# Kernel tuning notes

Hardware: AMD Instinct MI355X
Metric: run time of the kernel (lower is better)

## Reference

```python
import jax, jax.numpy as jnp
import numpy as np

B, N, DIN, DOUT, RATIO, K = 8, 4096, 128, 256, 4, 16
S = N // RATIO
BN_EPS = 1e-5


def furthest_point_sample(xyz, n_samples):
    # xyz: [B, N, 3] -> idx [B, n_samples] int32. Sequential farthest-distance reduction.
    b, n, _ = xyz.shape
    dist0 = jnp.full((b, n), 1e10, xyz.dtype)
    last0 = xyz[:, 0, :]  # first sampled point is index 0 (CUDA kernel convention)

    def step(carry, _):
        dist, last = carry
        d = jnp.sum((xyz - last[:, None, :]) ** 2, axis=-1)  # [B, N]
        dist = jnp.minimum(dist, d)
        nxt = jnp.argmax(dist, axis=1).astype(jnp.int32)      # [B]
        last = jnp.take_along_axis(xyz, nxt[:, None, None].astype(jnp.int32), axis=1)[:, 0, :]
        return (dist, last), nxt

    (_, _), idxs = jax.lax.scan(step, (dist0, last0), None, length=n_samples - 1)
    idx = jnp.concatenate([jnp.zeros((1, b), jnp.int32), idxs], axis=0).T  # [B, S]
    return idx


def knn_indices(query, points, k):
    # query [B,S,3], points [B,N,3] -> k nearest indices [B,S,k]
    q2 = jnp.sum(query ** 2, axis=-1)                           # [B,S]
    p2 = jnp.sum(points ** 2, axis=-1)                          # [B,N]
    d2 = q2[:, :, None] + p2[:, None, :] - 2.0 * jnp.einsum('bsd,bnd->bsn', query, points)
    _, idx = jax.lax.top_k(-d2, k)                              # smallest distances
    return idx


def setup_inputs() -> dict:
    key = jax.random.key(0)
    k1, k2, k3, k4 = jax.random.split(key, 4)
    input_feature = jax.random.normal(k1, (B, N, DIN), dtype=jnp.float32)
    xyz = jax.random.uniform(k2, (B, N, 3), dtype=jnp.float32)
    # linear params (torch nn.Linear: W [out,in], b [out])
    lim = 1.0 / np.sqrt(DIN)
    W = jax.random.uniform(k3, (DOUT, DIN), dtype=jnp.float32, minval=-lim, maxval=lim)
    b = jax.random.uniform(k4, (DOUT,), dtype=jnp.float32, minval=-lim, maxval=lim)
    gamma = jnp.ones((DOUT,), jnp.float32)
    beta = jnp.zeros((DOUT,), jnp.float32)
    return {"input_feature": input_feature, "xyz": xyz, "W": W, "b": b, "gamma": gamma, "beta": beta}


def reference(input_feature, xyz, W, b, gamma, beta):
    sample_idx = furthest_point_sample(xyz, S)                         # [B,S]
    sample_xyz = jnp.take_along_axis(xyz, sample_idx[:, :, None], axis=1)  # [B,S,3]
    knn_idx = knn_indices(sample_xyz, xyz, K)                          # [B,S,K]
    # gather_knn: [B,S,K,DIN]
    knn_feat = jax.vmap(lambda f, i: f[i])(input_feature, knn_idx)
    h = jnp.einsum('bskd,ed->bske', knn_feat, W) + b                   # linear [B,S,K,DOUT]
    # BatchNorm1d over channel dim, stats across (B, S*K) in training mode (biased var)
    mean = jnp.mean(h, axis=(0, 1, 2))
    var = jnp.var(h, axis=(0, 1, 2))
    h = gamma * (h - mean) * jax.lax.rsqrt(var + BN_EPS) + beta
    h = jax.nn.relu(h)
    sample_feature = jnp.max(h, axis=2)                                # [B,S,DOUT]
    return sample_feature, sample_xyz
```

## Files before the change

kernel.cpp:

```cpp
#include <hip/hip_runtime.h>
#include <hip/hip_bf16.h>

#define BB 8
#define NN 4096
#define DIN 128
#define DOUT 256
#define SS 1024
#define KK 16

__device__ float g_g[(size_t)BB * NN * DOUT];
__device__ int   g_knn[BB * SS * KK];
__device__ int   g_wcount[BB * NN];
__device__ float g_S1[DOUT];
__device__ float g_S2[DOUT];

typedef float f32x2 __attribute__((ext_vector_type(2)));

__device__ __forceinline__ unsigned long long umax64(unsigned long long a, unsigned long long b) {
    return a > b ? a : b;
}
__device__ __forceinline__ f32x2 pk_add(f32x2 a, f32x2 b) {
    f32x2 d; asm("v_pk_add_f32 %0, %1, %2" : "=v"(d) : "v"(a), "v"(b)); return d;
}
__device__ __forceinline__ f32x2 pk_mul(f32x2 a, f32x2 b) {
    f32x2 d; asm("v_pk_mul_f32 %0, %1, %2" : "=v"(d) : "v"(a), "v"(b)); return d;
}
__device__ __forceinline__ f32x2 pk_fma(f32x2 a, f32x2 b, f32x2 c) {
    f32x2 d; asm("v_pk_fma_f32 %0, %1, %2, %3" : "=v"(d) : "v"(a), "v"(b), "v"(c)); return d;
}

__global__ __launch_bounds__(512) void k_fused1(
    const float* __restrict__ feat, const float* __restrict__ xyz,
    const float* __restrict__ W, const float* __restrict__ bias,
    float* __restrict__ out)
{
    __shared__ __align__(16) float smem[16384];
    __shared__ __align__(16) unsigned long long swk64[2][8];

    if (blockIdx.x < BB) {
        #pragma clang fp contract(off)
        const int b = blockIdx.x, tid = threadIdx.x;
        const float* bx = xyz + (size_t)b * NN * 3;
        for (int i = 0; i < 8; ++i) {
            int p = tid + i * 512;
            float4 v; v.x = bx[p*3]; v.y = bx[p*3+1]; v.z = bx[p*3+2]; v.w = 0.f;
            ((float4*)smem)[p] = v;
        }
        __syncthreads();
        f32x2 px2[4], py2[4], pz2[4];
        double dist64[8];
        float thr[8];
        unsigned long long key[8];
        const int gbase = tid * 8;
        const unsigned long long D0 =
            ((unsigned long long)__double_as_longlong(1e10)) & ~0xFFFULL;
        const float THR0 = __uint_as_float(__float_as_uint(1e10f) + 16u);
        #pragma unroll
        for (int pp = 0; pp < 4; ++pp) {
            float4 v0 = ((float4*)smem)[gbase + 2*pp];
            float4 v1 = ((float4*)smem)[gbase + 2*pp + 1];
            px2[pp].x = v0.x; px2[pp].y = v1.x;
            py2[pp].x = v0.y; py2[pp].y = v1.y;
            pz2[pp].x = v0.z; pz2[pp].y = v1.z;
            dist64[2*pp]   = 1e10; dist64[2*pp+1] = 1e10;
            thr[2*pp] = THR0;      thr[2*pp+1] = THR0;
            key[2*pp]   = D0 | (unsigned long long)(4095 - (gbase + 2*pp));
            key[2*pp+1] = D0 | (unsigned long long)(4095 - (gbase + 2*pp + 1));
        }
        float4 c0v = ((float4*)smem)[0];
        float lxf = c0v.x, lyf = c0v.y, lzf = c0v.z;
        float* oxyz = out + (size_t)BB * SS * DOUT;
        if (tid == 0) {
            oxyz[(size_t)(b*SS)*3]   = lxf;
            oxyz[(size_t)(b*SS)*3+1] = lyf;
            oxyz[(size_t)(b*SS)*3+2] = lzf;
        }
        for (int s = 1; s < SS; ++s) {
            const double lxd = (double)lxf, lyd = (double)lyf, lzd = (double)lzf;
            f32x2 nlx; nlx.x = -lxf; nlx.y = -lxf;
            f32x2 nly; nly.x = -lyf; nly.y = -lyf;
            f32x2 nlz; nlz.x = -lzf; nlz.y = -lzf;
            #pragma unroll
            for (int pp = 0; pp < 4; ++pp) {
                f32x2 dx = pk_add(px2[pp], nlx);
                f32x2 dy = pk_add(py2[pp], nly);
                f32x2 dz = pk_add(pz2[pp], nlz);
                f32x2 d2 = pk_mul(dx, dx);
                d2 = pk_fma(dy, dy, d2);
                d2 = pk_fma(dz, dz, d2);
                if (d2.x < thr[2*pp]) {
                    const int r = 2*pp;
                    double ddx = (double)px2[pp].x - lxd;
                    double ddy = (double)py2[pp].x - lyd;
                    double ddz = (double)pz2[pp].x - lzd;
                    double m1 = ddx*ddx, m2 = ddy*ddy, m3 = ddz*ddz;
                    double d = (m1 + m2) + m3;
                    if (d < dist64[r]) {
                        dist64[r] = d;
                        thr[r] = __uint_as_float(__float_as_uint((float)d) + 16u);
                        key[r] = (((unsigned long long)__double_as_longlong(d)) & ~0xFFFULL)
                                 | (unsigned long long)(4095 - (gbase + r));
                    }
                }
                if (d2.y < thr[2*pp+1]) {
                    const int r = 2*pp + 1;
                    double ddx = (double)px2[pp].y - lxd;
                    double ddy = (double)py2[pp].y - lyd;
                    double ddz = (double)pz2[pp].y - lzd;
                    double m1 = ddx*ddx, m2 = ddy*ddy, m3 = ddz*ddz;
                    double d = (m1 + m2) + m3;
                    if (d < dist64[r]) {
                        dist64[r] = d;
                        thr[r] = __uint_as_float(__float_as_uint((float)d) + 16u);
                        key[r] = (((unsigned long long)__double_as_longlong(d)) & ~0xFFFULL)
                                 | (unsigned long long)(4095 - (gbase + r));
                    }
                }
            }
            unsigned long long kk;
            {
                unsigned long long a0 = umax64(key[0], key[1]);
                unsigned long long a1 = umax64(key[2], key[3]);
                unsigned long long a2 = umax64(key[4], key[5]);
                unsigned long long a3 = umax64(key[6], key[7]);
                kk = umax64(umax64(a0, a1), umax64(a2, a3));
            }
#define DPP64(CTRL) { \
    int _lo = __builtin_amdgcn_update_dpp(0, (int)(unsigned)kk, CTRL, 0xf, 0xf, true); \
    int _hi = __builtin_amdgcn_update_dpp(0, (int)(unsigned)(kk >> 32), CTRL, 0xf, 0xf, true); \
    unsigned long long _o = (((unsigned long long)(unsigned)_hi) << 32) | (unsigned)_lo; \
    if (_o > kk) kk = _o; }
            DPP64(0x111)
            DPP64(0x112)
            DPP64(0x114)
            DPP64(0x118)
            DPP64(0x142)
            DPP64(0x143)
#undef DPP64
            if ((tid & 63) == 63) swk64[s & 1][tid >> 6] = kk;
            __syncthreads();
            const unsigned long long* sw = swk64[s & 1];
            ulonglong2 s01 = ((const ulonglong2*)sw)[0];
            ulonglong2 s23 = ((const ulonglong2*)sw)[1];
            ulonglong2 s45 = ((const ulonglong2*)sw)[2];
            ulonglong2 s67 = ((const ulonglong2*)sw)[3];
            unsigned long long kmax = umax64(
                umax64(umax64(s01.x, s01.y), umax64(s23.x, s23.y)),
                umax64(umax64(s45.x, s45.y), umax64(s67.x, s67.y)));
            int widx = 4095 - (int)(kmax & 0xFFFULL);
            float4 c = ((float4*)smem)[widx];
            lxf = c.x; lyf = c.y; lzf = c.z;
            if (tid == 0) {
                oxyz[(size_t)(b*SS+s)*3]   = c.x;
                oxyz[(size_t)(b*SS+s)*3+1] = c.y;
                oxyz[(size_t)(b*SS+s)*3+2] = c.z;
            }
        }
    } else if (blockIdx.x < BB + 2048) {
        int gi = blockIdx.x - BB;
        int mt = gi & 511, nt = gi >> 9;
        int rbase = mt * 64, cbase = nt * 64;
        float* As = smem;
        float* Bs = smem + 64 * 36;
        int tid = threadIdx.x;
        int tx = tid & 15, ty = tid >> 4;
        int c0 = tx * 4, r0 = ty * 2;
        int lr = tid >> 3;
        int lk = (tid & 7) * 4;
        float acc[2][4] = {{0.f,0.f,0.f,0.f},{0.f,0.f,0.f,0.f}};
        for (int kc = 0; kc < 4; ++kc) {
            __syncthreads();
            float4 av = *(const float4*)&feat[(size_t)(rbase + lr) * DIN + kc*32 + lk];
            *(float4*)&As[lr * 36 + lk] = av;
            float4 wv = *(const float4*)&W[(size_t)(cbase + lr) * DIN + kc*32 + lk];
            Bs[(lk+0)*68 + lr] = wv.x;
            Bs[(lk+1)*68 + lr] = wv.y;
            Bs[(lk+2)*68 + lr] = wv.z;
            Bs[(lk+3)*68 + lr] = wv.w;
            __syncthreads();
            const float* Ar0 = &As[r0 * 36];
            const float* Ar1 = Ar0 + 36;
            #pragma unroll
            for (int k = 0; k < 32; ++k) {
                float a0 = Ar0[k], a1 = Ar1[k];
                float4 bv = *(float4*)&Bs[k * 68 + c0];
                acc[0][0] += a0 * bv.x; acc[0][1] += a0 * bv.y;
                acc[0][2] += a0 * bv.z; acc[0][3] += a0 * bv.w;
                acc[1][0] += a1 * bv.x; acc[1][1] += a1 * bv.y;
                acc[1][2] += a1 * bv.z; acc[1][3] += a1 * bv.w;
            }
        }
        float4 bb4 = *(const float4*)&bias[cbase + c0];
        float4 o0, o1;
        o0.x = acc[0][0] + bb4.x; o0.y = acc[0][1] + bb4.y;
        o0.z = acc[0][2] + bb4.z; o0.w = acc[0][3] + bb4.w;
        o1.x = acc[1][0] + bb4.x; o1.y = acc[1][1] + bb4.y;
        o1.z = acc[1][2] + bb4.z; o1.w = acc[1][3] + bb4.w;
        *(float4*)&g_g[(size_t)(rbase + r0)     * DOUT + cbase + c0] = o0;
        *(float4*)&g_g[(size_t)(rbase + r0 + 1) * DOUT + cbase + c0] = o1;
    } else {
        int zi = blockIdx.x - (BB + 2048);
        int t = zi * 512 + threadIdx.x;
        g_wcount[t] = 0;
        g_wcount[t + 16384] = 0;
        if (t < DOUT) { g_S1[t] = 0.f; g_S2[t] = 0.f; }
    }
}

__global__ __launch_bounds__(1024) void k_knn(
    const float* __restrict__ xyz, const float* __restrict__ out)
{
    __shared__ __align__(16) float4 pts[NN];
    __shared__ unsigned hist[16][512];
    __shared__ int cand[16][128];
    __shared__ int cnt[16];
    const int tid = threadIdx.x, lane = tid & 63, w = tid >> 6;
    const int q = blockIdx.x * 16 + w;
    const int b = blockIdx.x >> 6;
    const float* bx = xyz + (size_t)b * NN * 3;
    for (int i = 0; i < 4; ++i) {
        int p = tid + i * 1024;
        float4 v; v.x = bx[p*3]; v.y = bx[p*3+1]; v.z = bx[p*3+2]; v.w = 0.f;
        pts[p] = v;
    }
    { unsigned* h = &hist[0][0];
      #pragma unroll
      for (int i = 0; i < 8; ++i) h[tid + i * 1024] = 0u; }
    if (tid < 16) cnt[tid] = 0;
    __syncthreads();

    const float* sx = out + (size_t)BB * SS * DOUT + (size_t)q * 3;
    const float qxf = sx[0], qyf = sx[1], qzf = sx[2];
    unsigned minub = 0xFFFFFFFFu;
    for (int t = 0; t < 64; ++t) {
        int n = t * 64 + lane;
        float4 p = pts[n];
        float dx = qxf - p.x, dy = qyf - p.y, dz = qzf - p.z;
        float df = fmaf(dz, dz, fmaf(dy, dy, dx * dx));
        unsigned ub = __float_as_uint(df);
        minub = ub < minub ? ub : minub;
        unsigned bk = ub < 0x30800000u ? 0u : ((ub - 0x30800000u) >> 19);
        bk = bk > 511u ? 511u : bk;
        atomicAdd(&hist[w][bk], 1u);
    }
    #pragma unroll
    for (int m = 1; m < 64; m <<= 1) {
        unsigned o = __shfl_xor(minub, m);
        minub = o < minub ? o : minub;
    }
    unsigned mb = minub < 0x30800000u ? 0u : ((minub - 0x30800000u) >> 19);
    mb = mb > 511u ? 511u : mb;
    int Tb = 511;
    unsigned base = 0;
    for (int ch = (int)(mb >> 6); ch < 8; ++ch) {
        unsigned v = hist[w][ch * 64 + lane];
        #pragma unroll
        for (int m = 1; m < 64; m <<= 1) {
            unsigned t2 = __shfl_up(v, m);
            if (lane >= m) v += t2;
        }
        unsigned tot = __shfl(v, 63);
        unsigned long long msk = __ballot(base + v >= 16u);
        if (msk) { Tb = ch * 64 + (__ffsll(msk) - 1); break; }
        base += tot;
    }
    unsigned Tcap = (unsigned)Tb + 1u; Tcap = Tcap > 511u ? 511u : Tcap;
    for (int t = 0; t < 64; ++t) {
        int n = t * 64 + lane;
        float4 p = pts[n];
        float dx = qxf - p.x, dy = qyf - p.y, dz = qzf - p.z;
        float df = fmaf(dz, dz, fmaf(dy, dy, dx * dx));
        unsigned ub = __float_as_uint(df);
        unsigned bk = ub < 0x30800000u ? 0u : ((ub - 0x30800000u) >> 19);
        bk = bk > 511u ? 511u : bk;
        if (bk <= Tcap) {
            int slot = atomicAdd(&cnt[w], 1);
            if (slot < 128) cand[w][slot] = n;
        }
    }
    {
        #pragma clang fp contract(off)
        int count = cnt[w]; count = count > 128 ? 128 : count;
        const double qx = (double)qxf, qy = (double)qyf, qz = (double)qzf;
        int i0 = lane < count ? cand[w][lane] : -1;
        int i1 = (lane + 64) < count ? cand[w][lane + 64] : -1;
        double d0 = 1e300, d1 = 1e300;
        if (i0 >= 0) {
            float4 p = pts[i0];
            double dx = qx - (double)p.x, dy = qy - (double)p.y, dz = qz - (double)p.z;
            double m1 = dx*dx, m2 = dy*dy, m3 = dz*dz;
            d0 = (m1 + m2) + m3;
        }
        if (i1 >= 0) {
            float4 p = pts[i1];
            double dx = qx - (double)p.x, dy = qy - (double)p.y, dz = qz - (double)p.z;
            double m1 = dx*dx, m2 = dy*dy, m3 = dz*dz;
            d1 = (m1 + m2) + m3;
        }
        int r0 = 0, r1 = 0;
        for (int i = 0; i < count; ++i) {
            double od; int oi;
            if (i < 64) { od = __shfl(d0, i);      oi = __shfl(i0, i); }
            else        { od = __shfl(d1, i - 64); oi = __shfl(i1, i - 64); }
            if ((od < d0) || (od == d0 && oi < i0)) ++r0;
            if ((od < d1) || (od == d1 && oi < i1)) ++r1;
        }
        if (i0 >= 0 && r0 < KK) {
            g_knn[(size_t)q * KK + r0] = i0;
            atomicAdd(&g_wcount[b * NN + i0], 1);
        }
        if (i1 >= 0 && r1 < KK) {
            g_knn[(size_t)q * KK + r1] = i1;
            atomicAdd(&g_wcount[b * NN + i1], 1);
        }
    }
}

__global__ __launch_bounds__(256) void k_stats()
{
    int tid = threadIdx.x;
    int rbase = blockIdx.x * 128;
    float a1 = 0.f, a2 = 0.f;
    for (int i = 0; i < 128; ++i) {
        int row = rbase + i;
        int w = g_wcount[row];
        if (w) {
            float v = g_g[(size_t)row * DOUT + tid];
            float wf = (float)w;
            a1 += wf * v;
            a2 += wf * v * v;
        }
    }
    atomicAdd(&g_S1[tid], a1);
    atomicAdd(&g_S2[tid], a2);
}

__global__ __launch_bounds__(256) void k_final(
    const float* __restrict__ gamma, const float* __restrict__ beta,
    float* __restrict__ out)
{
    int w = threadIdx.x >> 6, lane = threadIdx.x & 63;
    int q = blockIdx.x * 4 + w;
    int b = q >> 10;
    int c = lane * 4;
    const int* ki = g_knn + (size_t)q * KK;
    float4 m; m.x = m.y = m.z = m.w = -1e30f;
    for (int k = 0; k < KK; ++k) {
        int idx = ki[k];
        float4 v = *(const float4*)&g_g[((size_t)(b * NN + idx)) * DOUT + c];
        m.x = fmaxf(m.x, v.x); m.y = fmaxf(m.y, v.y);
        m.z = fmaxf(m.z, v.z); m.w = fmaxf(m.w, v.w);
    }
    const float inv = 1.0f / 131072.0f;
    float4 s1 = *(const float4*)&g_S1[c];
    float4 s2 = *(const float4*)&g_S2[c];
    float4 ga = *(const float4*)&gamma[c];
    float4 be = *(const float4*)&beta[c];
    float4 o;
    {
        float mean = s1.x * inv; float var = s2.x * inv - mean * mean;
        float rs = rsqrtf(var + 1e-5f);
        float t = ga.x * (m.x - mean); t = t * rs; t += be.x; o.x = fmaxf(t, 0.f);
    }
    {
        float mean = s1.y * inv; float var = s2.y * inv - mean * mean;
        float rs = rsqrtf(var + 1e-5f);
        float t = ga.y * (m.y - mean); t = t * rs; t += be.y; o.y = fmaxf(t, 0.f);
    }
    {
        float mean = s1.z * inv; float var = s2.z * inv - mean * mean;
        float rs = rsqrtf(var + 1e-5f);
        float t = ga.z * (m.z - mean); t = t * rs; t += be.z; o.z = fmaxf(t, 0.f);
    }
    {
        float mean = s1.w * inv; float var = s2.w * inv - mean * mean;
        float rs = rsqrtf(var + 1e-5f);
        float t = ga.w * (m.w - mean); t = t * rs; t += be.w; o.w = fmaxf(t, 0.f);
    }
    *(float4*)&out[(size_t)q * DOUT + c] = o;
}

extern "C" void kernel_launch(void* const* d_in, const int* in_sizes, int n_in,
                              void* d_out, int out_size, void* d_ws, size_t ws_size,
                              hipStream_t stream) {
    (void)in_sizes; (void)n_in; (void)out_size; (void)d_ws; (void)ws_size;
    const float* feat  = (const float*)d_in[0];
    const float* xyz   = (const float*)d_in[1];
    const float* W     = (const float*)d_in[2];
    const float* bias  = (const float*)d_in[3];
    const float* gamma = (const float*)d_in[4];
    const float* beta  = (const float*)d_in[5];
    float* out = (float*)d_out;

    k_fused1<<<BB + 2048 + 32, 512, 0, stream>>>(feat, xyz, W, bias, out);
    k_knn   <<<BB * SS / 16, 1024, 0, stream>>>(xyz, out);
    k_stats <<<256, 256, 0, stream>>>();
    k_final <<<2048, 256, 0, stream>>>(gamma, beta, out);
}
```

Baseline: 1.012 ms.

## Widen FPS blocks to 1024 threads with four points per thread

```diff
diff --git a/kernel.cpp b/kernel.cpp
--- a/kernel.cpp
+++ b/kernel.cpp
@@ -28,35 +28,38 @@
 __device__ __forceinline__ f32x2 pk_fma(f32x2 a, f32x2 b, f32x2 c) {
     f32x2 d; asm("v_pk_fma_f32 %0, %1, %2, %3" : "=v"(d) : "v"(a), "v"(b), "v"(c)); return d;
 }
-
-__global__ __launch_bounds__(512) void k_fused1(
+__device__ __forceinline__ void lgkm_barrier() {
+    asm volatile("s_waitcnt lgkmcnt(0)\n\ts_barrier" ::: "memory");
+}
+
+__global__ __launch_bounds__(1024) void k_fused1(
     const float* __restrict__ feat, const float* __restrict__ xyz,
     const float* __restrict__ W, const float* __restrict__ bias,
     float* __restrict__ out)
 {
     __shared__ __align__(16) float smem[16384];
-    __shared__ __align__(16) unsigned long long swk64[2][8];
+    __shared__ __align__(16) unsigned long long swk64[2][16];
 
     if (blockIdx.x < BB) {
         #pragma clang fp contract(off)
         const int b = blockIdx.x, tid = threadIdx.x;
         const float* bx = xyz + (size_t)b * NN * 3;
-        for (int i = 0; i < 8; ++i) {
-            int p = tid + i * 512;
+        for (int i = 0; i < 4; ++i) {
+            int p = tid + i * 1024;
             float4 v; v.x = bx[p*3]; v.y = bx[p*3+1]; v.z = bx[p*3+2]; v.w = 0.f;
             ((float4*)smem)[p] = v;
         }
         __syncthreads();
-        f32x2 px2[4], py2[4], pz2[4];
-        double dist64[8];
-        float thr[8];
-        unsigned long long key[8];
-        const int gbase = tid * 8;
+        f32x2 px2[2], py2[2], pz2[2];
+        double dist64[4];
+        float thr[4];
+        unsigned long long key[4];
+        const int gbase = tid * 4;
         const unsigned long long D0 =
             ((unsigned long long)__double_as_longlong(1e10)) & ~0xFFFULL;
         const float THR0 = __uint_as_float(__float_as_uint(1e10f) + 16u);
         #pragma unroll
-        for (int pp = 0; pp < 4; ++pp) {
+        for (int pp = 0; pp < 2; ++pp) {
             float4 v0 = ((float4*)smem)[gbase + 2*pp];
             float4 v1 = ((float4*)smem)[gbase + 2*pp + 1];
             px2[pp].x = v0.x; px2[pp].y = v1.x;
@@ -76,12 +79,13 @@
             oxyz[(size_t)(b*SS)*3+2] = lzf;
         }
         for (int s = 1; s < SS; ++s) {
+            const int sl = s & 1;
             const double lxd = (double)lxf, lyd = (double)lyf, lzd = (double)lzf;
             f32x2 nlx; nlx.x = -lxf; nlx.y = -lxf;
             f32x2 nly; nly.x = -lyf; nly.y = -lyf;
             f32x2 nlz; nlz.x = -lzf; nlz.y = -lzf;
             #pragma unroll
-            for (int pp = 0; pp < 4; ++pp) {
+            for (int pp = 0; pp < 2; ++pp) {
                 f32x2 dx = pk_add(px2[pp], nlx);
                 f32x2 dy = pk_add(py2[pp], nly);
                 f32x2 dz = pk_add(pz2[pp], nlz);
@@ -117,14 +121,8 @@
                     }
                 }
             }
-            unsigned long long kk;
-            {
-                unsigned long long a0 = umax64(key[0], key[1]);
-                unsigned long long a1 = umax64(key[2], key[3]);
-                unsigned long long a2 = umax64(key[4], key[5]);
-                unsigned long long a3 = umax64(key[6], key[7]);
-                kk = umax64(umax64(a0, a1), umax64(a2, a3));
-            }
+            unsigned long long kk = umax64(umax64(key[0], key[1]),
+                                           umax64(key[2], key[3]));
 #define DPP64(CTRL) { \
     int _lo = __builtin_amdgcn_update_dpp(0, (int)(unsigned)kk, CTRL, 0xf, 0xf, true); \
     int _hi = __builtin_amdgcn_update_dpp(0, (int)(unsigned)(kk >> 32), CTRL, 0xf, 0xf, true); \
@@ -137,16 +135,22 @@
             DPP64(0x142)
             DPP64(0x143)
 #undef DPP64
-            if ((tid & 63) == 63) swk64[s & 1][tid >> 6] = kk;
-            __syncthreads();
-            const unsigned long long* sw = swk64[s & 1];
-            ulonglong2 s01 = ((const ulonglong2*)sw)[0];
-            ulonglong2 s23 = ((const ulonglong2*)sw)[1];
-            ulonglong2 s45 = ((const ulonglong2*)sw)[2];
-            ulonglong2 s67 = ((const ulonglong2*)sw)[3];
-            unsigned long long kmax = umax64(
-                umax64(umax64(s01.x, s01.y), umax64(s23.x, s23.y)),
-                umax64(umax64(s45.x, s45.y), umax64(s67.x, s67.y)));
+            if ((tid & 63) == 63) swk64[sl][tid >> 6] = kk;
+            lgkm_barrier();
+            const unsigned long long* sw = swk64[sl];
+            ulonglong2 q0 = ((const ulonglong2*)sw)[0];
+            ulonglong2 q1 = ((const ulonglong2*)sw)[1];
+            ulonglong2 q2 = ((const ulonglong2*)sw)[2];
+            ulonglong2 q3 = ((const ulonglong2*)sw)[3];
+            ulonglong2 q4 = ((const ulonglong2*)sw)[4];
+            ulonglong2 q5 = ((const ulonglong2*)sw)[5];
+            ulonglong2 q6 = ((const ulonglong2*)sw)[6];
+            ulonglong2 q7 = ((const ulonglong2*)sw)[7];
+            unsigned long long m0 = umax64(umax64(q0.x, q0.y), umax64(q1.x, q1.y));
+            unsigned long long m1 = umax64(umax64(q2.x, q2.y), umax64(q3.x, q3.y));
+            unsigned long long m2 = umax64(umax64(q4.x, q4.y), umax64(q5.x, q5.y));
+            unsigned long long m3 = umax64(umax64(q6.x, q6.y), umax64(q7.x, q7.y));
+            unsigned long long kmax = umax64(umax64(m0, m1), umax64(m2, m3));
             int widx = 4095 - (int)(kmax & 0xFFFULL);
             float4 c = ((float4*)smem)[widx];
             lxf = c.x; lyf = c.y; lzf = c.z;
@@ -163,46 +167,52 @@
         float* As = smem;
         float* Bs = smem + 64 * 36;
         int tid = threadIdx.x;
-        int tx = tid & 15, ty = tid >> 4;
+        bool active = tid < 512;
+        int tx = tid & 15, ty = (tid & 511) >> 4;
         int c0 = tx * 4, r0 = ty * 2;
-        int lr = tid >> 3;
+        int lr = (tid & 511) >> 3;
         int lk = (tid & 7) * 4;
         float acc[2][4] = {{0.f,0.f,0.f,0.f},{0.f,0.f,0.f,0.f}};
         for (int kc = 0; kc < 4; ++kc) {
             __syncthreads();
-            float4 av = *(const float4*)&feat[(size_t)(rbase + lr) * DIN + kc*32 + lk];
-            *(float4*)&As[lr * 36 + lk] = av;
-            float4 wv = *(const float4*)&W[(size_t)(cbase + lr) * DIN + kc*32 + lk];
-            Bs[(lk+0)*68 + lr] = wv.x;
-            Bs[(lk+1)*68 + lr] = wv.y;
-            Bs[(lk+2)*68 + lr] = wv.z;
-            Bs[(lk+3)*68 + lr] = wv.w;
+            if (active) {
+                float4 av = *(const float4*)&feat[(size_t)(rbase + lr) * DIN + kc*32 + lk];
+                *(float4*)&As[lr * 36 + lk] = av;
+                float4 wv = *(const float4*)&W[(size_t)(cbase + lr) * DIN + kc*32 + lk];
+                Bs[(lk+0)*68 + lr] = wv.x;
+                Bs[(lk+1)*68 + lr] = wv.y;
+                Bs[(lk+2)*68 + lr] = wv.z;
+                Bs[(lk+3)*68 + lr] = wv.w;
+            }
             __syncthreads();
-            const float* Ar0 = &As[r0 * 36];
-            const float* Ar1 = Ar0 + 36;
-            #pragma unroll
-            for (int k = 0; k < 32; ++k) {
-                float a0 = Ar0[k], a1 = Ar1[k];
-                float4 bv = *(float4*)&Bs[k * 68 + c0];
-                acc[0][0] += a0 * bv.x; acc[0][1] += a0 * bv.y;
-                acc[0][2] += a0 * bv.z; acc[0][3] += a0 * bv.w;
-                acc[1][0] += a1 * bv.x; acc[1][1] += a1 * bv.y;
-                acc[1][2] += a1 * bv.z; acc[1][3] += a1 * bv.w;
+            if (active) {
+                const float* Ar0 = &As[r0 * 36];
+                const float* Ar1 = Ar0 + 36;
+                #pragma unroll
+                for (int k = 0; k < 32; ++k) {
+                    float a0 = Ar0[k], a1 = Ar1[k];
+                    float4 bv = *(float4*)&Bs[k * 68 + c0];
+                    acc[0][0] += a0 * bv.x; acc[0][1] += a0 * bv.y;
+                    acc[0][2] += a0 * bv.z; acc[0][3] += a0 * bv.w;
+                    acc[1][0] += a1 * bv.x; acc[1][1] += a1 * bv.y;
+                    acc[1][2] += a1 * bv.z; acc[1][3] += a1 * bv.w;
+                }
             }
         }
-        float4 bb4 = *(const float4*)&bias[cbase + c0];
-        float4 o0, o1;
-        o0.x = acc[0][0] + bb4.x; o0.y = acc[0][1] + bb4.y;
-        o0.z = acc[0][2] + bb4.z; o0.w = acc[0][3] + bb4.w;
-        o1.x = acc[1][0] + bb4.x; o1.y = acc[1][1] + bb4.y;
-        o1.z = acc[1][2] + bb4.z; o1.w = acc[1][3] + bb4.w;
-        *(float4*)&g_g[(size_t)(rbase + r0)     * DOUT + cbase + c0] = o0;
-        *(float4*)&g_g[(size_t)(rbase + r0 + 1) * DOUT + cbase + c0] = o1;
+        if (active) {
+            float4 bb4 = *(const float4*)&bias[cbase + c0];
+            float4 o0, o1;
+            o0.x = acc[0][0] + bb4.x; o0.y = acc[0][1] + bb4.y;
+            o0.z = acc[0][2] + bb4.z; o0.w = acc[0][3] + bb4.w;
+            o1.x = acc[1][0] + bb4.x; o1.y = acc[1][1] + bb4.y;
+            o1.z = acc[1][2] + bb4.z; o1.w = acc[1][3] + bb4.w;
+            *(float4*)&g_g[(size_t)(rbase + r0)     * DOUT + cbase + c0] = o0;
+            *(float4*)&g_g[(size_t)(rbase + r0 + 1) * DOUT + cbase + c0] = o1;
+        }
     } else {
         int zi = blockIdx.x - (BB + 2048);
-        int t = zi * 512 + threadIdx.x;
+        int t = zi * 1024 + threadIdx.x;
         g_wcount[t] = 0;
-        g_wcount[t + 16384] = 0;
         if (t < DOUT) { g_S1[t] = 0.f; g_S2[t] = 0.f; }
     }
 }
@@ -392,7 +402,7 @@
     const float* beta  = (const float*)d_in[5];
     float* out = (float*)d_out;
 
-    k_fused1<<<BB + 2048 + 32, 512, 0, stream>>>(feat, xyz, W, bias, out);
+    k_fused1<<<BB + 2048 + 32, 1024, 0, stream>>>(feat, xyz, W, bias, out);
     k_knn   <<<BB * SS / 16, 1024, 0, stream>>>(xyz, out);
     k_stats <<<256, 256, 0, stream>>>();
     k_final <<<2048, 256, 0, stream>>>(gamma, beta, out);
```

After: 1.289 ms. 1.27x slower.
